# Kernel optimization log

Hardware: AMD Instinct MI355X
Metric: run time of the kernel (lower is better)

The kernel has to match this reference:

```python
import jax, jax.numpy as jnp
import numpy as np

D_MODEL = 256
N_LEVELS = 4
N_HEADS = 8
N_POINTS = 4
HEAD_DIM = D_MODEL // N_HEADS
SPATIAL_SHAPES = np.array([[128, 128], [64, 64], [32, 32], [16, 16]], dtype=np.int64)
LEN_IN = int((SPATIAL_SHAPES[:, 0] * SPATIAL_SHAPES[:, 1]).sum())  # 21760
BATCH = 2
LEN_Q = LEN_IN  # encoder self-attention


def setup_inputs() -> dict:
    key = jax.random.key(0)
    ks = jax.random.split(key, 12)
    C = D_MODEL
    lvl_start = np.concatenate([[0], np.cumsum(SPATIAL_SHAPES[:, 0] * SPATIAL_SHAPES[:, 1])[:-1]]).astype(np.int64)
    return {
        'query': jax.random.normal(ks[0], (BATCH, LEN_Q, C), jnp.float32),
        'reference_points': jax.random.uniform(ks[1], (BATCH, LEN_Q, N_LEVELS, 2), jnp.float32),
        'input_flatten': jax.random.normal(ks[2], (BATCH, LEN_IN, C), jnp.float32),
        'input_spatial_shapes': SPATIAL_SHAPES,          # static numpy: shapes must be concrete
        'input_level_start_index': lvl_start,            # static numpy
        'Wv': jax.random.normal(ks[3], (C, C), jnp.float32) / np.sqrt(C),
        'bv': jnp.zeros((C,), jnp.float32),
        'Woff': jax.random.normal(ks[4], (C, N_HEADS * N_LEVELS * N_POINTS * 2), jnp.float32) * 0.01,
        'boff': jax.random.normal(ks[5], (N_HEADS * N_LEVELS * N_POINTS * 2,), jnp.float32) * 0.5,
        'Wa': jax.random.normal(ks[6], (C, N_HEADS * N_LEVELS * N_POINTS), jnp.float32) * 0.01,
        'ba': jnp.zeros((N_HEADS * N_LEVELS * N_POINTS,), jnp.float32),
        'Wo': jax.random.normal(ks[7], (C, C), jnp.float32) / np.sqrt(C),
        'bo': jnp.zeros((C,), jnp.float32),
    }


def _grid_sample_bilinear(v, grid):
    """v: (B,H,W,D); grid: (B,Q,P,2) in [-1,1] (x,y). align_corners=False, zero padding."""
    B, H, W, D = v.shape
    x = (grid[..., 0] + 1.0) * 0.5 * W - 0.5
    y = (grid[..., 1] + 1.0) * 0.5 * H - 0.5
    x0 = jnp.floor(x)
    y0 = jnp.floor(y)
    wx = x - x0
    wy = y - y0
    b = jnp.arange(B)[:, None, None]

    def corner(xi, yi, w):
        valid = (xi >= 0) & (xi < W) & (yi >= 0) & (yi < H)
        xi_ = jnp.clip(xi, 0, W - 1).astype(jnp.int32)
        yi_ = jnp.clip(yi, 0, H - 1).astype(jnp.int32)
        return v[b, yi_, xi_] * (w * valid)[..., None]  # (B,Q,P,D)

    return (corner(x0, y0, (1 - wx) * (1 - wy))
            + corner(x0 + 1, y0, wx * (1 - wy))
            + corner(x0, y0 + 1, (1 - wx) * wy)
            + corner(x0 + 1, y0 + 1, wx * wy))


def _msdeform_attn(query, reference_points, input_flatten, spatial_shapes_np,
                   Wv, bv, Woff, boff, Wa, ba, Wo, bo):
    N, Lq, C = query.shape
    Lin = input_flatten.shape[1]
    M, L, P, D = N_HEADS, N_LEVELS, N_POINTS, HEAD_DIM

    value = (input_flatten @ Wv + bv).reshape(N, Lin, M, D)
    offsets = (query @ Woff + boff).reshape(N, Lq, M, L, P, 2)
    attn = jax.nn.softmax((query @ Wa + ba).reshape(N, Lq, M, L * P), axis=-1).reshape(N, Lq, M, L, P)

    # sampling locations in [0,1] -> grid in [-1,1]
    grids = 2.0 * (reference_points[:, :, None, :, None, :] + offsets) - 1.0  # (N,Lq,M,L,P,2)

    out = jnp.zeros((N * M, Lq, D), value.dtype)
    start = 0
    for lid in range(L):
        H_, W_ = int(spatial_shapes_np[lid, 0]), int(spatial_shapes_np[lid, 1])
        v_l = value[:, start:start + H_ * W_]                       # (N,HW,M,D)
        v_l = v_l.transpose(0, 2, 1, 3).reshape(N * M, H_, W_, D)   # (N*M,H,W,D)
        g_l = grids[:, :, :, lid].transpose(0, 2, 1, 3, 4).reshape(N * M, Lq, P, 2)
        sampled = _grid_sample_bilinear(v_l, g_l)                   # (N*M,Lq,P,D)
        a_l = attn[:, :, :, lid].transpose(0, 2, 1, 3).reshape(N * M, Lq, P)
        out = out + jnp.einsum('bqpd,bqp->bqd', sampled, a_l)
        start += H_ * W_

    out = out.reshape(N, M, Lq, D).transpose(0, 2, 1, 3).reshape(N, Lq, M * D)
    return out @ Wo + bo


def reference(query, reference_points, input_flatten, input_spatial_shapes,
              input_level_start_index, Wv, bv, Woff, boff, Wa, ba, Wo, bo):
    spatial_np = np.asarray(input_spatial_shapes)
    return _msdeform_attn(query, reference_points, input_flatten, spatial_np,
                          Wv, bv, Woff, boff, Wa, ba, Wo, bo)
```

## Files before the change

kernel.cpp:

```cpp
#include <hip/hip_runtime.h>
#include <cstdint>
#include <cstddef>

#define LEN_IN  21760
#define BATCH   2
#define MROWS   (BATCH * LEN_IN)

typedef _Float16 hv8 __attribute__((ext_vector_type(8)));
typedef float    fv4 __attribute__((ext_vector_type(4)));

#define WAIT_LGKM0() __builtin_amdgcn_s_waitcnt(0xC07F)
#define RAW_BARRIER() __builtin_amdgcn_s_barrier()

__global__ __launch_bounds__(256) void cvt_weights(
    const float* __restrict__ Wv, const float* __restrict__ Woff,
    const float* __restrict__ Wa, const float* __restrict__ Wo,
    _Float16* __restrict__ WvT, _Float16* __restrict__ WoffT2,
    _Float16* __restrict__ WaT, _Float16* __restrict__ WoT)
{
  __shared__ float t[64][65];
  const int id = blockIdx.x, tid = threadIdx.x;
  const int c = tid & 63, r4 = tid >> 6;

  const float* src; _Float16* dst; int N; bool split = false; int nt, kt;
  if (id < 16)      { src = Wv;   dst = WvT;    N = 256; nt = id & 3;        kt = id >> 2; }
  else if (id < 32) { src = Woff; dst = WoffT2; N = 256; nt = (id - 16) & 3; kt = (id - 16) >> 2; split = true; }
  else if (id < 40) { src = Wa;   dst = WaT;    N = 128; nt = (id - 32) & 1; kt = (id - 32) >> 1; }
  else              { src = Wo;   dst = WoT;    N = 256; nt = (id - 40) & 3; kt = (id - 40) >> 2; }
  const int nb = nt * 64, kb = kt * 64;

#pragma unroll
  for (int rr = 0; rr < 16; ++rr) {
    const int r = rr * 4 + r4;
    t[r][c] = src[(size_t)(kb + r) * N + nb + c];
  }
  __syncthreads();
#pragma unroll
  for (int rr = 0; rr < 16; ++rr) {
    const int r = rr * 4 + r4;
    const float v = t[c][r];
    const _Float16 h = (_Float16)v;
    dst[(size_t)(nb + r) * 256 + kb + c] = h;
    if (split)
      dst[(size_t)(256 + nb + r) * 256 + kb + c] = (_Float16)(v - (float)h);
  }
}

template<int NTOT, int AF32, int OUTMODE>
__global__ __launch_bounds__(256) void gemm_pipe(
    const void* __restrict__ Ap, const _Float16* __restrict__ Bt,
    const float* __restrict__ bias, void* __restrict__ Cout)
{
  __shared__ _Float16 As[2][64 * 40];
  __shared__ _Float16 Bs[2][128 * 40];

  const int tid = threadIdx.x, lane = tid & 63, wave = tid >> 6;
  const int l15 = lane & 15, quad = lane >> 4;
  const int wc = wave * 32;
  const int rowBase = blockIdx.x * 64;
  const int colBase = blockIdx.y * 128;
  const int rs = tid >> 2, ks = (tid & 3) * 8;

  const float*    A32 = (const float*)Ap;
  const _Float16* A16 = (const _Float16*)Ap;

  float4 pa[3][2]; hv8 pa16[3]; hv8 pb[2][2];

  auto issueA = [&](int it) {
    const int k0 = it * 32, s = it % 3;
    if constexpr (AF32) {
      pa[s][0] = *(const float4*)&A32[(size_t)(rowBase + rs) * 256 + k0 + ks];
      pa[s][1] = *(const float4*)&A32[(size_t)(rowBase + rs) * 256 + k0 + ks + 4];
    } else {
      pa16[s] = *(const hv8*)&A16[(size_t)(rowBase + rs) * 256 + k0 + ks];
    }
  };
  auto issueB = [&](int it) {
    const int k0 = it * 32, s = it & 1;
#pragma unroll
    for (int p = 0; p < 2; ++p)
      pb[s][p] = *(const hv8*)&Bt[(size_t)(colBase + p * 64 + rs) * 256 + k0 + ks];
  };

  issueA(0); issueB(0); issueA(1); issueB(1); issueA(2);

  fv4 acc[4][2] = {};

#pragma unroll
  for (int it = 0; it < 8; ++it) {
    const int sb = it & 1, sa = it % 3;
    if constexpr (AF32) {
      const float4 f0 = pa[sa][0], f1 = pa[sa][1];
      const float fa[8] = {f0.x, f0.y, f0.z, f0.w, f1.x, f1.y, f1.z, f1.w};
      hv8 h;
#pragma unroll
      for (int e = 0; e < 8; ++e) h[e] = (_Float16)fa[e];
      *(hv8*)&As[sb][rs * 40 + ks] = h;
    } else {
      *(hv8*)&As[sb][rs * 40 + ks] = pa16[sa];
    }
#pragma unroll
    for (int p = 0; p < 2; ++p)
      *(hv8*)&Bs[sb][(p * 64 + rs) * 40 + ks] = pb[sb][p];
    if (it + 2 < 8) issueB(it + 2);
    if (it + 3 < 8) issueA(it + 3);
    WAIT_LGKM0();
    RAW_BARRIER();

    hv8 af[4];
#pragma unroll
    for (int i = 0; i < 4; ++i)
      af[i] = *(const hv8*)&As[sb][(i * 16 + l15) * 40 + quad * 8];
#pragma unroll
    for (int j = 0; j < 2; ++j) {
      const hv8 bf = *(const hv8*)&Bs[sb][(wc + j * 16 + l15) * 40 + quad * 8];
#pragma unroll
      for (int i = 0; i < 4; ++i)
        acc[i][j] = __builtin_amdgcn_mfma_f32_16x16x32_f16(af[i], bf, acc[i][j], 0, 0, 0);
    }
  }

#pragma unroll
  for (int j = 0; j < 2; ++j) {
    const int col = colBase + wc + j * 16 + l15;
    const float bj = bias[col];
#pragma unroll
    for (int i = 0; i < 4; ++i)
#pragma unroll
      for (int rg = 0; rg < 4; ++rg) {
        const int row = rowBase + i * 16 + quad * 4 + rg;
        const float v = acc[i][j][rg] + bj;
        if constexpr (OUTMODE == 0) {
          ((float*)Cout)[(size_t)row * NTOT + col] = v;
        } else if constexpr (OUTMODE == 1) {
          ((_Float16*)Cout)[(size_t)row * NTOT + col] = (_Float16)v;
        } else {
          const int n = (row >= LEN_IN) ? 1 : 0;
          const int pix = row - n * LEN_IN;
          const int m = col >> 5, d = col & 31;
          ((_Float16*)Cout)[((size_t)(n * 8 + m) * LEN_IN + pix) * 32 + d] = (_Float16)v;
        }
      }
  }
}

__global__ __launch_bounds__(256) void gemm_offs_logits(
    const float* __restrict__ A, const _Float16* __restrict__ B2,
    const float* __restrict__ boff, const float* __restrict__ ba,
    const float* __restrict__ refpts,
    float* __restrict__ C, _Float16* __restrict__ logits16)
{
  __shared__ _Float16 Ash[64 * 40], Asl[64 * 40];
  __shared__ _Float16 Bs[256 * 40];

  const bool offs = (blockIdx.y < 2);
  const int np = offs ? 4 : 2;
  const int tid = threadIdx.x, lane = tid & 63, wave = tid >> 6;
  const int l15 = lane & 15, quad = lane >> 4;
  const int wc = wave * 32;
  const int rowBase = blockIdx.x * 64;
  const int colBase = offs ? blockIdx.y * 128 : 0;
  const int rs = tid >> 2, ks = (tid & 3) * 8;

  float4 pa[3][2]; hv8 pb[2][4];

  auto issueA = [&](int it) {
    const int k0 = it * 32, s = it % 3;
    pa[s][0] = *(const float4*)&A[(size_t)(rowBase + rs) * 256 + k0 + ks];
    pa[s][1] = *(const float4*)&A[(size_t)(rowBase + rs) * 256 + k0 + ks + 4];
  };
  auto issueB = [&](int it) {
    const int k0 = it * 32, s = it & 1;
#pragma unroll
    for (int p = 0; p < 4; ++p) {
      if (p >= np) break;
      const int grow = offs
          ? ((p < 2) ? (colBase + p * 64 + rs) : (256 + colBase + (p - 2) * 64 + rs))
          : (512 + p * 64 + rs);
      pb[s][p] = *(const hv8*)&B2[(size_t)grow * 256 + k0 + ks];
    }
  };

  issueA(0); issueB(0); issueA(1); issueB(1); issueA(2);

  fv4 acc[4][2] = {};

#pragma unroll
  for (int it = 0; it < 8; ++it) {
    const int sa = it % 3, s2 = it & 1;
    {
      const float4 f0 = pa[sa][0], f1 = pa[sa][1];
      const float fa[8] = {f0.x, f0.y, f0.z, f0.w, f1.x, f1.y, f1.z, f1.w};
      hv8 hh, ll;
#pragma unroll
      for (int e = 0; e < 8; ++e) {
        hh[e] = (_Float16)fa[e];
        ll[e] = (_Float16)(fa[e] - (float)hh[e]);
      }
      *(hv8*)&Ash[rs * 40 + ks] = hh;
      if (offs) *(hv8*)&Asl[rs * 40 + ks] = ll;
    }
#pragma unroll
    for (int p = 0; p < 4; ++p) {
      if (p >= np) break;
      *(hv8*)&Bs[(p * 64 + rs) * 40 + ks] = pb[s2][p];
    }
    if (it + 2 < 8) issueB(it + 2);
    if (it + 3 < 8) issueA(it + 3);
    WAIT_LGKM0();
    RAW_BARRIER();

    hv8 ah[4];
#pragma unroll
    for (int i = 0; i < 4; ++i)
      ah[i] = *(const hv8*)&Ash[(i * 16 + l15) * 40 + quad * 8];

    if (offs) {
      hv8 al[4];
#pragma unroll
      for (int i = 0; i < 4; ++i)
        al[i] = *(const hv8*)&Asl[(i * 16 + l15) * 40 + quad * 8];
#pragma unroll
      for (int j = 0; j < 2; ++j) {
        const hv8 bh = *(const hv8*)&Bs[(wc + j * 16 + l15) * 40 + quad * 8];
        const hv8 bl = *(const hv8*)&Bs[(128 + wc + j * 16 + l15) * 40 + quad * 8];
#pragma unroll
        for (int i = 0; i < 4; ++i) {
          acc[i][j] = __builtin_amdgcn_mfma_f32_16x16x32_f16(ah[i], bh, acc[i][j], 0, 0, 0);
          acc[i][j] = __builtin_amdgcn_mfma_f32_16x16x32_f16(ah[i], bl, acc[i][j], 0, 0, 0);
          acc[i][j] = __builtin_amdgcn_mfma_f32_16x16x32_f16(al[i], bh, acc[i][j], 0, 0, 0);
        }
      }
    } else {
#pragma unroll
      for (int j = 0; j < 2; ++j) {
        const hv8 bh = *(const hv8*)&Bs[(wc + j * 16 + l15) * 40 + quad * 8];
#pragma unroll
        for (int i = 0; i < 4; ++i)
          acc[i][j] = __builtin_amdgcn_mfma_f32_16x16x32_f16(ah[i], bh, acc[i][j], 0, 0, 0);
      }
    }
    WAIT_LGKM0();
    RAW_BARRIER();
  }

  if (offs) {
#pragma unroll
    for (int j = 0; j < 2; ++j) {
      const int c = colBase + wc + j * 16 + l15;
      const int xy = c & 1, l = (c >> 3) & 3;
      const float Wl = (float)(128 >> l);
      const float bj = boff[c];
#pragma unroll
      for (int i = 0; i < 4; ++i)
#pragma unroll
        for (int rg = 0; rg < 4; ++rg) {
          const int row = rowBase + i * 16 + quad * 4 + rg;
          const float ref = refpts[(size_t)row * 8 + l * 2 + xy];
          C[(size_t)row * 256 + c] = (acc[i][j][rg] + bj + ref) * Wl - 0.5f;
        }
    }
  } else {
#pragma unroll
    for (int j = 0; j < 2; ++j) {
      const int col = wc + j * 16 + l15;
      const float bj = ba[col];
#pragma unroll
      for (int i = 0; i < 4; ++i)
#pragma unroll
        for (int rg = 0; rg < 4; ++rg) {
          const int row = rowBase + i * 16 + quad * 4 + rg;
          logits16[(size_t)row * 128 + col] = (_Float16)(acc[i][j][rg] + bj);
        }
    }
  }
}

__global__ __launch_bounds__(256, 8) void sample_kernel(
    const _Float16* __restrict__ value16,
    const float* __restrict__ coords,
    const _Float16* __restrict__ logits16,
    _Float16* __restrict__ outp16)
{
  __shared__ unsigned s_pair[4096];
  __shared__ float    s_attn[1024];

  const int tid = threadIdx.x;
  const int qBase = blockIdx.x * 8;

  if (tid < 64) {
    const hv8* lp = (const hv8*)&logits16[(size_t)(qBase + (tid >> 3)) * 128 + (tid & 7) * 16];
    const hv8 w0 = lp[0], w1 = lp[1];
    float w[16];
#pragma unroll
    for (int e = 0; e < 8; ++e) { w[e] = (float)w0[e]; w[8 + e] = (float)w1[e]; }
    float mx = w[0];
#pragma unroll
    for (int i = 1; i < 16; ++i) mx = fmaxf(mx, w[i]);
    float sum = 0.f;
#pragma unroll
    for (int i = 0; i < 16; ++i) { w[i] = expf(w[i] - mx); sum += w[i]; }
    const float inv = 1.f / sum;
#pragma unroll
    for (int p = 0; p < 16; ++p) s_attn[p * 64 + tid] = w[p] * inv;
  }
  __syncthreads();

#pragma unroll
  for (int k = 0; k < 4; ++k) {
    const int i = tid + 256 * k;
    const int p = i >> 6, q = (i >> 3) & 7, m = i & 7;
    const int l = p >> 2, pp = p & 3;
    const int qg = qBase + q;
    const float2 of = *(const float2*)&coords[(size_t)qg * 256 + ((m * 4 + l) * 4 + pp) * 2];
    const float aw = s_attn[i];
    const int W = 128 >> l;
    const int st = (l == 0) ? 0 : (l == 1) ? 16384 : (l == 2) ? 20480 : 21504;
    const float xf = floorf(of.x), yf = floorf(of.y);
    const int x0 = (int)xf, y0 = (int)yf;
    const float wx = of.x - xf, wy = of.y - yf;
    uint4 rec;
    unsigned* rp = &rec.x;
#pragma unroll
    for (int c = 0; c < 4; ++c) {
      const int dx = c & 1, dy = c >> 1;
      const int xi = x0 + dx, yi = y0 + dy;
      const bool valid = (xi >= 0) & (xi < W) & (yi >= 0) & (yi < W);
      const float w = (dx ? wx : 1.f - wx) * (dy ? wy : 1.f - wy) * aw;
      union { _Float16 h; unsigned short s; } pk;
      pk.h = (_Float16)w;
      const unsigned idx = (unsigned)(st + yi * W + xi);
      rp[c] = valid ? (idx | ((unsigned)pk.s << 16)) : 0u;
    }
    *(uint4*)&s_pair[i * 4] = rec;
  }
  __syncthreads();

  const int wave = tid >> 6, lane = tid & 63;
  const int qloc = wave * 2 + (lane >> 5);
  const int sub = lane & 31, m = sub >> 2, j = sub & 3;
  const int qg = qBase + qloc;
  const int n = (qg >= LEN_IN) ? 1 : 0;
  const char* base = (const char*)value16 + (size_t)(n * 8 + m) * LEN_IN * 64 + j * 16;
  const int lb = qloc * 8 + m;

  float acc8[8] = {0.f, 0.f, 0.f, 0.f, 0.f, 0.f, 0.f, 0.f};
#pragma unroll 4
  for (int p = 0; p < 16; ++p) {
    const uint4 u4 = *(const uint4*)&s_pair[(p * 64 + lb) * 4];
    const unsigned uu[4] = {u4.x, u4.y, u4.z, u4.w};
#pragma unroll
    for (int c = 0; c < 4; ++c) {
      const unsigned u = uu[c];
      union { unsigned short s; _Float16 h; } pk;
      pk.s = (unsigned short)(u >> 16);
      const float w = (float)pk.h;
      const hv8 v = *(const hv8*)(base + (size_t)(u & 32767u) * 64);
#pragma unroll
      for (int e = 0; e < 8; ++e) acc8[e] = fmaf(w, (float)v[e], acc8[e]);
    }
  }

  hv8 o;
#pragma unroll
  for (int e = 0; e < 8; ++e) o[e] = (_Float16)acc8[e];
  *(hv8*)&outp16[(size_t)qg * 256 + m * 32 + j * 8] = o;
}

extern "C" void kernel_launch(void* const* d_in, const int* in_sizes, int n_in,
                              void* d_out, int out_size, void* d_ws, size_t ws_size,
                              hipStream_t stream) {
  const float* query   = (const float*)d_in[0];
  const float* refpts  = (const float*)d_in[1];
  const float* flatten = (const float*)d_in[2];
  const float* Wv   = (const float*)d_in[5];
  const float* bv   = (const float*)d_in[6];
  const float* Woff = (const float*)d_in[7];
  const float* boff = (const float*)d_in[8];
  const float* Wa   = (const float*)d_in[9];
  const float* ba   = (const float*)d_in[10];
  const float* Wo   = (const float*)d_in[11];
  const float* bo   = (const float*)d_in[12];
  float* out = (float*)d_out;

  const size_t NE = (size_t)MROWS * 256;
  _Float16* value16  = (_Float16*)d_ws;
  float*    coords   = (float*)(value16 + NE);
  _Float16* logits16 = (_Float16*)(coords + NE);
  _Float16* outp16   = logits16 + NE / 2;
  _Float16* WvT      = outp16 + NE;
  _Float16* WoffT2   = WvT + 256 * 256;
  _Float16* WaT      = WoffT2 + 512 * 256;
  _Float16* WoT      = WaT + 128 * 256;

  const dim3 blk(256);
  const int mtiles = MROWS / 64;

  cvt_weights<<<dim3(56), blk, 0, stream>>>(Wv, Woff, Wa, Wo, WvT, WoffT2, WaT, WoT);

  gemm_pipe<256, 1, 2><<<dim3(mtiles, 2), blk, 0, stream>>>(flatten, WvT, bv, value16);
  gemm_offs_logits<<<dim3(mtiles, 3), blk, 0, stream>>>(query, WoffT2, boff, ba, refpts,
                                                        coords, logits16);
  sample_kernel<<<dim3(MROWS / 8), blk, 0, stream>>>(value16, coords, logits16, outp16);
  gemm_pipe<256, 0, 0><<<dim3(mtiles, 2), blk, 0, stream>>>(outp16, WoT, bo, out);
}
```

Measured before the change: 276.6 us.

## Replace LDS-staged pipelined GEMMs with direct global-to-register MFMA operand loads

Removes LDS staging, software prefetch pipelining and barriers from the projection GEMMs and the offset/logit GEMM. Each wave now loads its MFMA A and B fragments straight from global memory, relying on L1/L2 caching for reuse across waves. This drops the barrier and LDS traffic cost, but every wave re-reads the shared A rows and loses explicit latency hiding from the prefetch pipeline. It also produces strided 16-byte loads per lane instead of coalesced tile loads.

```diff
diff --git a/kernel.cpp b/kernel.cpp
--- a/kernel.cpp
+++ b/kernel.cpp
@@ -8,9 +8,6 @@
 
 typedef _Float16 hv8 __attribute__((ext_vector_type(8)));
 typedef float    fv4 __attribute__((ext_vector_type(4)));
-
-#define WAIT_LGKM0() __builtin_amdgcn_s_waitcnt(0xC07F)
-#define RAW_BARRIER() __builtin_amdgcn_s_barrier()
 
 __global__ __launch_bounds__(256) void cvt_weights(
     const float* __restrict__ Wv, const float* __restrict__ Woff,
@@ -47,73 +44,46 @@
 }
 
 template<int NTOT, int AF32, int OUTMODE>
-__global__ __launch_bounds__(256) void gemm_pipe(
+__global__ __launch_bounds__(256) void gemm_direct(
     const void* __restrict__ Ap, const _Float16* __restrict__ Bt,
     const float* __restrict__ bias, void* __restrict__ Cout)
 {
-  __shared__ _Float16 As[2][64 * 40];
-  __shared__ _Float16 Bs[2][128 * 40];
-
   const int tid = threadIdx.x, lane = tid & 63, wave = tid >> 6;
   const int l15 = lane & 15, quad = lane >> 4;
   const int wc = wave * 32;
   const int rowBase = blockIdx.x * 64;
   const int colBase = blockIdx.y * 128;
-  const int rs = tid >> 2, ks = (tid & 3) * 8;
 
   const float*    A32 = (const float*)Ap;
   const _Float16* A16 = (const _Float16*)Ap;
 
-  float4 pa[3][2]; hv8 pa16[3]; hv8 pb[2][2];
-
-  auto issueA = [&](int it) {
-    const int k0 = it * 32, s = it % 3;
-    if constexpr (AF32) {
-      pa[s][0] = *(const float4*)&A32[(size_t)(rowBase + rs) * 256 + k0 + ks];
-      pa[s][1] = *(const float4*)&A32[(size_t)(rowBase + rs) * 256 + k0 + ks + 4];
-    } else {
-      pa16[s] = *(const hv8*)&A16[(size_t)(rowBase + rs) * 256 + k0 + ks];
-    }
-  };
-  auto issueB = [&](int it) {
-    const int k0 = it * 32, s = it & 1;
-#pragma unroll
-    for (int p = 0; p < 2; ++p)
-      pb[s][p] = *(const hv8*)&Bt[(size_t)(colBase + p * 64 + rs) * 256 + k0 + ks];
-  };
-
-  issueA(0); issueB(0); issueA(1); issueB(1); issueA(2);
-
   fv4 acc[4][2] = {};
 
 #pragma unroll
   for (int it = 0; it < 8; ++it) {
-    const int sb = it & 1, sa = it % 3;
-    if constexpr (AF32) {
-      const float4 f0 = pa[sa][0], f1 = pa[sa][1];
-      const float fa[8] = {f0.x, f0.y, f0.z, f0.w, f1.x, f1.y, f1.z, f1.w};
-      hv8 h;
-#pragma unroll
-      for (int e = 0; e < 8; ++e) h[e] = (_Float16)fa[e];
-      *(hv8*)&As[sb][rs * 40 + ks] = h;
-    } else {
-      *(hv8*)&As[sb][rs * 40 + ks] = pa16[sa];
-    }
-#pragma unroll
-    for (int p = 0; p < 2; ++p)
-      *(hv8*)&Bs[sb][(p * 64 + rs) * 40 + ks] = pb[sb][p];
-    if (it + 2 < 8) issueB(it + 2);
-    if (it + 3 < 8) issueA(it + 3);
-    WAIT_LGKM0();
-    RAW_BARRIER();
+    const int k0 = it * 32 + quad * 8;
 
     hv8 af[4];
 #pragma unroll
-    for (int i = 0; i < 4; ++i)
-      af[i] = *(const hv8*)&As[sb][(i * 16 + l15) * 40 + quad * 8];
+    for (int i = 0; i < 4; ++i) {
+      const size_t rowoff = (size_t)(rowBase + i * 16 + l15) * 256 + k0;
+      if constexpr (AF32) {
+        const float4 f0 = *(const float4*)&A32[rowoff];
+        const float4 f1 = *(const float4*)&A32[rowoff + 4];
+        hv8 h;
+        h[0] = (_Float16)f0.x; h[1] = (_Float16)f0.y;
+        h[2] = (_Float16)f0.z; h[3] = (_Float16)f0.w;
+        h[4] = (_Float16)f1.x; h[5] = (_Float16)f1.y;
+        h[6] = (_Float16)f1.z; h[7] = (_Float16)f1.w;
+        af[i] = h;
+      } else {
+        af[i] = *(const hv8*)&A16[rowoff];
+      }
+    }
+
 #pragma unroll
     for (int j = 0; j < 2; ++j) {
-      const hv8 bf = *(const hv8*)&Bs[sb][(wc + j * 16 + l15) * 40 + quad * 8];
+      const hv8 bf = *(const hv8*)&Bt[(size_t)(colBase + wc + j * 16 + l15) * 256 + k0];
 #pragma unroll
       for (int i = 0; i < 4; ++i)
         acc[i][j] = __builtin_amdgcn_mfma_f32_16x16x32_f16(af[i], bf, acc[i][j], 0, 0, 0);
@@ -150,46 +120,25 @@
     const float* __restrict__ refpts,
     float* __restrict__ C, _Float16* __restrict__ logits16)
 {
-  __shared__ _Float16 Ash[64 * 40], Asl[64 * 40];
-  __shared__ _Float16 Bs[256 * 40];
-
   const bool offs = (blockIdx.y < 2);
-  const int np = offs ? 4 : 2;
   const int tid = threadIdx.x, lane = tid & 63, wave = tid >> 6;
   const int l15 = lane & 15, quad = lane >> 4;
   const int wc = wave * 32;
   const int rowBase = blockIdx.x * 64;
   const int colBase = offs ? blockIdx.y * 128 : 0;
-  const int rs = tid >> 2, ks = (tid & 3) * 8;
-
-  float4 pa[3][2]; hv8 pb[2][4];
-
-  auto issueA = [&](int it) {
-    const int k0 = it * 32, s = it % 3;
-    pa[s][0] = *(const float4*)&A[(size_t)(rowBase + rs) * 256 + k0 + ks];
-    pa[s][1] = *(const float4*)&A[(size_t)(rowBase + rs) * 256 + k0 + ks + 4];
-  };
-  auto issueB = [&](int it) {
-    const int k0 = it * 32, s = it & 1;
-#pragma unroll
-    for (int p = 0; p < 4; ++p) {
-      if (p >= np) break;
-      const int grow = offs
-          ? ((p < 2) ? (colBase + p * 64 + rs) : (256 + colBase + (p - 2) * 64 + rs))
-          : (512 + p * 64 + rs);
-      pb[s][p] = *(const hv8*)&B2[(size_t)grow * 256 + k0 + ks];
-    }
-  };
-
-  issueA(0); issueB(0); issueA(1); issueB(1); issueA(2);
 
   fv4 acc[4][2] = {};
 
 #pragma unroll
   for (int it = 0; it < 8; ++it) {
-    const int sa = it % 3, s2 = it & 1;
-    {
-      const float4 f0 = pa[sa][0], f1 = pa[sa][1];
+    const int k0 = it * 32 + quad * 8;
+
+    hv8 ah[4], al[4];
+#pragma unroll
+    for (int i = 0; i < 4; ++i) {
+      const size_t rowoff = (size_t)(rowBase + i * 16 + l15) * 256 + k0;
+      const float4 f0 = *(const float4*)&A[rowoff];
+      const float4 f1 = *(const float4*)&A[rowoff + 4];
       const float fa[8] = {f0.x, f0.y, f0.z, f0.w, f1.x, f1.y, f1.z, f1.w};
       hv8 hh, ll;
 #pragma unroll
@@ -197,33 +146,15 @@
         hh[e] = (_Float16)fa[e];
         ll[e] = (_Float16)(fa[e] - (float)hh[e]);
       }
-      *(hv8*)&Ash[rs * 40 + ks] = hh;
-      if (offs) *(hv8*)&Asl[rs * 40 + ks] = ll;
-    }
-#pragma unroll
-    for (int p = 0; p < 4; ++p) {
-      if (p >= np) break;
-      *(hv8*)&Bs[(p * 64 + rs) * 40 + ks] = pb[s2][p];
-    }
-    if (it + 2 < 8) issueB(it + 2);
-    if (it + 3 < 8) issueA(it + 3);
-    WAIT_LGKM0();
-    RAW_BARRIER();
-
-    hv8 ah[4];
-#pragma unroll
-    for (int i = 0; i < 4; ++i)
-      ah[i] = *(const hv8*)&Ash[(i * 16 + l15) * 40 + quad * 8];
+      ah[i] = hh; al[i] = ll;
+    }
 
     if (offs) {
-      hv8 al[4];
-#pragma unroll
-      for (int i = 0; i < 4; ++i)
-        al[i] = *(const hv8*)&Asl[(i * 16 + l15) * 40 + quad * 8];
 #pragma unroll
       for (int j = 0; j < 2; ++j) {
-        const hv8 bh = *(const hv8*)&Bs[(wc + j * 16 + l15) * 40 + quad * 8];
-        const hv8 bl = *(const hv8*)&Bs[(128 + wc + j * 16 + l15) * 40 + quad * 8];
+        const int colr = colBase + wc + j * 16 + l15;
+        const hv8 bh = *(const hv8*)&B2[(size_t)colr * 256 + k0];
+        const hv8 bl = *(const hv8*)&B2[(size_t)(256 + colr) * 256 + k0];
 #pragma unroll
         for (int i = 0; i < 4; ++i) {
           acc[i][j] = __builtin_amdgcn_mfma_f32_16x16x32_f16(ah[i], bh, acc[i][j], 0, 0, 0);
@@ -234,14 +165,12 @@
     } else {
 #pragma unroll
       for (int j = 0; j < 2; ++j) {
-        const hv8 bh = *(const hv8*)&Bs[(wc + j * 16 + l15) * 40 + quad * 8];
+        const hv8 bh = *(const hv8*)&B2[(size_t)(512 + wc + j * 16 + l15) * 256 + k0];
 #pragma unroll
         for (int i = 0; i < 4; ++i)
           acc[i][j] = __builtin_amdgcn_mfma_f32_16x16x32_f16(ah[i], bh, acc[i][j], 0, 0, 0);
       }
     }
-    WAIT_LGKM0();
-    RAW_BARRIER();
   }
 
   if (offs) {
@@ -398,9 +327,9 @@
 
   cvt_weights<<<dim3(56), blk, 0, stream>>>(Wv, Woff, Wa, Wo, WvT, WoffT2, WaT, WoT);
 
-  gemm_pipe<256, 1, 2><<<dim3(mtiles, 2), blk, 0, stream>>>(flatten, WvT, bv, value16);
+  gemm_direct<256, 1, 2><<<dim3(mtiles, 2), blk, 0, stream>>>(flatten, WvT, bv, value16);
   gemm_offs_logits<<<dim3(mtiles, 3), blk, 0, stream>>>(query, WoffT2, boff, ba, refpts,
                                                         coords, logits16);
   sample_kernel<<<dim3(MROWS / 8), blk, 0, stream>>>(value16, coords, logits16, outp16);
-  gemm_pipe<256, 0, 0><<<dim3(mtiles, 2), blk, 0, stream>>>(outp16, WoT, bo, out);
-}
+  gemm_direct<256, 0, 0><<<dim3(mtiles, 2), blk, 0, stream>>>(outp16, WoT, bo, out);
+}
```

Result: slower. 380.8 us (+37.6%).
